# Performance work log

Hardware: AMD Instinct MI355X
Metric: run time of the kernel (lower is better)

The kernel has to match this reference:

```python
import jax, jax.numpy as jnp
import numpy as np

K = 7            # involution kernel size
GC = 16          # group_channels (fixed in module)
BN_EPS = 1e-5


def setup_inputs() -> dict:
    key = jax.random.key(0)
    ks = jax.random.split(key, 9)
    B, C, H, W = 4, 256, 64, 64
    OUT = 256
    CR = C // 4                     # reduction_ratio = 4
    G = C // GC                     # groups = 16
    x = jax.random.normal(ks[0], (B, C, H, W), dtype=jnp.float32)
    # conv1: 1x1 conv C -> C//4, no bias (followed by BN)
    w1 = jax.random.normal(ks[1], (CR, C), dtype=jnp.float32) * (1.0 / np.sqrt(C))
    gamma = jax.random.uniform(ks[2], (CR,), dtype=jnp.float32, minval=0.5, maxval=1.5)
    beta = jax.random.normal(ks[3], (CR,), dtype=jnp.float32) * 0.1
    mean = jax.random.normal(ks[4], (CR,), dtype=jnp.float32) * 0.1
    var = jax.random.uniform(ks[5], (CR,), dtype=jnp.float32, minval=0.5, maxval=1.5)
    # conv2: 1x1 conv C//4 -> K^2 * groups, with bias
    w2 = jax.random.normal(ks[6], (K * K * G, CR), dtype=jnp.float32) * (1.0 / np.sqrt(CR))
    b2 = jax.random.normal(ks[7], (K * K * G,), dtype=jnp.float32) * 0.01
    # pointwise: 1x1 conv C -> OUT, no bias
    wp = jax.random.normal(ks[8], (OUT, C), dtype=jnp.float32) * (1.0 / np.sqrt(C))
    return {"x": x, "w1": w1, "gamma": gamma, "beta": beta, "mean": mean,
            "var": var, "w2": w2, "b2": b2, "wp": wp}


def reference(x, w1, gamma, beta, mean, var, w2, b2, wp):
    b, c, h, w = x.shape
    groups = c // GC
    # weight-generation branch: 1x1 conv -> BN (inference) -> ReLU -> 1x1 conv
    y = jnp.einsum('oc,bchw->bohw', w1, x)
    scale = (gamma * jax.lax.rsqrt(var + BN_EPS))[None, :, None, None]
    y = jax.nn.relu((y - mean[None, :, None, None]) * scale + beta[None, :, None, None])
    wt = jnp.einsum('oc,bchw->bohw', w2, y) + b2[None, :, None, None]
    wt = wt.reshape(b, groups, 1, K * K, h, w)
    # unfold: (b, c*K*K, h, w) with channel-major ordering (matches torch Unfold)
    p = (K - 1) // 2
    patches = jax.lax.conv_general_dilated_patches(
        x, (K, K), (1, 1), ((p, p), (p, p)))
    patches = patches.reshape(b, groups, GC, K * K, h, w)
    out = (wt * patches).sum(axis=3).reshape(b, c, h, w)
    return jnp.einsum('oc,bchw->bohw', wp, out)
```

## Files before the change

kernel.cpp:

```cpp
#include <hip/hip_runtime.h>

typedef __attribute__((ext_vector_type(8))) short bf16x8;
typedef __attribute__((ext_vector_type(4))) float f32x4;
typedef __attribute__((ext_vector_type(8))) _Float16 h16x8;
typedef unsigned short u16;
typedef unsigned int u32;

__device__ __forceinline__ float bf2f(u16 u) {
    u32 x = ((u32)u) << 16;
    return __builtin_bit_cast(float, x);
}
__device__ __forceinline__ u16 f2bf(float f) {
    u32 x = __builtin_bit_cast(u32, f);
    return (u16)((x + 0x7fffu + ((x >> 16) & 1u)) >> 16);
}
__device__ __forceinline__ u16 f2h(float f) {
    _Float16 h = (_Float16)f;
    return __builtin_bit_cast(u16, h);
}
__device__ __forceinline__ u32 bfpair_to_h2(u32 a) {
    float f0 = bf2f((u16)(a & 0xffffu));
    float f1 = bf2f((u16)(a >> 16));
    return (u32)f2h(f0) | ((u32)f2h(f1) << 16);
}

__global__ __launch_bounds__(256) void prep2_k(
    const float* __restrict__ x,
    const float* __restrict__ w1, const float* __restrict__ gamma,
    const float* __restrict__ beta, const float* __restrict__ mean,
    const float* __restrict__ var, const float* __restrict__ w2,
    const float* __restrict__ wp,
    u16* __restrict__ xpk, u16* __restrict__ w1pk, float* __restrict__ b1,
    u16* __restrict__ w2gpk, u16* __restrict__ wppk)
{
    const int t = threadIdx.x;
    const int blk = blockIdx.x;
    if (blk < 2048) {
        const int b = blk >> 9, kg = (blk >> 4) & 31, pb = blk & 15;
        const int pix = pb * 256 + t;
        const float* xb = x + ((size_t)(b * 256 + kg * 8)) * 4096 + pix;
        u16 p[8];
#pragma unroll
        for (int j = 0; j < 8; ++j) p[j] = f2bf(xb[(size_t)j * 4096]);
        uint4 v;
        v.x = (u32)p[0] | ((u32)p[1] << 16);
        v.y = (u32)p[2] | ((u32)p[3] << 16);
        v.z = (u32)p[4] | ((u32)p[5] << 16);
        v.w = (u32)p[6] | ((u32)p[7] << 16);
        *reinterpret_cast<uint4*>(&xpk[(((size_t)b * 32 + kg) * 4096 + pix) * 8]) = v;
        return;
    }
    int idx = (blk - 2048) * 256 + t;
    if (idx < 16384) {
        int kg = idx >> 9, m = (idx >> 3) & 63, j = idx & 7;
        float s = gamma[m] * rsqrtf(var[m] + 1e-5f);
        w1pk[idx] = f2bf(w1[m * 256 + kg * 8 + j] * s);
    } else if (idx < 16448) {
        int o = idx - 16384;
        float s = gamma[o] * rsqrtf(var[o] + 1e-5f);
        b1[o] = beta[o] - mean[o] * s;
    } else if (idx < 81984) {
        int i = idx - 16448;
        int g = i >> 12, kg = (i >> 9) & 7, m = (i >> 3) & 63, j = i & 7;
        w2gpk[i] = (m < 49) ? f2bf(w2[(g * 49 + m) * 64 + kg * 8 + j]) : (u16)0;
    } else if (idx < 147520) {
        int i = idx - 81984;
        int kg = i >> 11, m = (i >> 3) & 255, j = i & 7;
        wppk[i] = f2bf(wp[m * 256 + kg * 8 + j]);
    }
}

__global__ __launch_bounds__(256) void gemm1m_k(
    const u16* __restrict__ xpk, const u16* __restrict__ w1pk,
    const float* __restrict__ b1, u16* __restrict__ ypk)
{
    __shared__ u16 Ws[32 * 64 * 8];
    __shared__ u16 As[2][8 * 64 * 8];

    const int t = threadIdx.x, lane = t & 63, wave = t >> 6;
    const int b = blockIdx.y, n0 = blockIdx.x * 64;
    const int ln = lane & 15, lk = lane >> 4;
    const u16* Ab = xpk + (size_t)b * 32 * 4096 * 8;

    for (int s = t; s < 2048; s += 256) {
        int kg = s >> 6, m = s & 63;
        uint4 v = *reinterpret_cast<const uint4*>(&w1pk[(size_t)s * 8]);
        *reinterpret_cast<uint4*>(&Ws[((kg * 64) + (m ^ (kg & 7))) * 8]) = v;
    }
    uint4 rs[2];
#pragma unroll
    for (int r = 0; r < 2; ++r) {
        int s = r * 256 + t, kg = s >> 6, nn = s & 63;
        rs[r] = *reinterpret_cast<const uint4*>(&Ab[((size_t)kg * 4096 + n0 + nn) * 8]);
    }
#pragma unroll
    for (int r = 0; r < 2; ++r) {
        int s = r * 256 + t, kg = s >> 6, nn = s & 63;
        *reinterpret_cast<uint4*>(&As[0][((kg * 64) + (nn ^ kg)) * 8]) = rs[r];
    }
    __syncthreads();

    f32x4 acc[4];
#pragma unroll
    for (int i = 0; i < 4; ++i)
#pragma unroll
        for (int e = 0; e < 4; ++e) acc[i][e] = 0.f;

    for (int ks = 0; ks < 4; ++ks) {
        const int cur = ks & 1;
        if (ks < 3) {
#pragma unroll
            for (int r = 0; r < 2; ++r) {
                int s = r * 256 + t, kg = s >> 6, nn = s & 63;
                rs[r] = *reinterpret_cast<const uint4*>(
                    &Ab[(((size_t)(ks + 1) * 8 + kg) * 4096 + n0 + nn) * 8]);
            }
        }
#pragma unroll
        for (int k32 = 0; k32 < 2; ++k32) {
            const int kgl = k32 * 4 + lk;
            const int kgw = ks * 8 + kgl;
            bf16x8 a[4];
#pragma unroll
            for (int i = 0; i < 4; ++i) {
                int n = i * 16 + ln;
                a[i] = *reinterpret_cast<const bf16x8*>(
                    &As[cur][((kgl * 64) + (n ^ kgl)) * 8]);
            }
            const int m = wave * 16 + ln;
            const bf16x8 bfr = *reinterpret_cast<const bf16x8*>(
                &Ws[((kgw * 64) + (m ^ (kgw & 7))) * 8]);
#pragma unroll
            for (int i = 0; i < 4; ++i)
                acc[i] = __builtin_amdgcn_mfma_f32_16x16x32_bf16(a[i], bfr, acc[i], 0, 0, 0);
        }
        if (ks < 3) {
#pragma unroll
            for (int r = 0; r < 2; ++r) {
                int s = r * 256 + t, kg = s >> 6, nn = s & 63;
                *reinterpret_cast<uint4*>(
                    &As[cur ^ 1][((kg * 64) + (nn ^ kg)) * 8]) = rs[r];
            }
            __syncthreads();
        }
    }

    const int m = wave * 16 + ln;
    const float bv = b1[m];
    u16* yb = ypk + ((size_t)b * 8 + (m >> 3)) * 4096 * 8 + (m & 7);
#pragma unroll
    for (int i = 0; i < 4; ++i) {
        const int n = n0 + i * 16 + lk * 4;
#pragma unroll
        for (int r = 0; r < 4; ++r)
            yb[(size_t)(n + r) * 8] = f2bf(fmaxf(acc[i][r] + bv, 0.f));
    }
}

__global__ __launch_bounds__(256, 2) void fusedinv_k(
    const u16* __restrict__ ypk, const u16* __restrict__ w2gpk,
    const float* __restrict__ b2, const u16* __restrict__ xpk,
    u16* __restrict__ invpk)
{
    __shared__ alignas(16) char Lds[66560];
    u16* As = (u16*)Lds;
    u16* Ws = (u16*)(Lds + 32768);
    _Float16* xs = (_Float16*)Lds;
    u16* wt16 = (u16*)(Lds + 40960);

    const int t = threadIdx.x, lane = t & 63, wave = t >> 6;
    const int tile = blockIdx.x, g = blockIdx.y, b = blockIdx.z;
    const int ty0 = (tile >> 2) * 16, tx0 = (tile & 3) * 16;
    const int ln = lane & 15, lk = lane >> 4;

    const u16* yb = ypk + (size_t)b * 8 * 4096 * 8;
#pragma unroll
    for (int r = 0; r < 8; ++r) {
        int s = r * 256 + t;
        int kg = s >> 8, n = s & 255;
        int gpix = (ty0 + (n >> 4)) * 64 + tx0 + (n & 15);
        *reinterpret_cast<uint4*>(&As[(size_t)s * 8]) =
            *reinterpret_cast<const uint4*>(&yb[((size_t)kg * 4096 + gpix) * 8]);
    }
#pragma unroll
    for (int r = 0; r < 2; ++r) {
        int s = r * 256 + t;
        *reinterpret_cast<uint4*>(&Ws[(size_t)s * 8]) =
            *reinterpret_cast<const uint4*>(&w2gpk[((size_t)g * 512 + s) * 8]);
    }
    __syncthreads();

    f32x4 acc[16];
#pragma unroll
    for (int i = 0; i < 16; ++i)
#pragma unroll
        for (int e = 0; e < 4; ++e) acc[i][e] = 0.f;

#pragma unroll
    for (int k32 = 0; k32 < 2; ++k32) {
        const int kg = k32 * 4 + lk;
        const bf16x8 wf = *reinterpret_cast<const bf16x8*>(
            &Ws[((kg * 64) + wave * 16 + ln) * 8]);
#pragma unroll
        for (int i = 0; i < 16; ++i) {
            const bf16x8 af = *reinterpret_cast<const bf16x8*>(
                &As[((kg * 256) + i * 16 + ln) * 8]);
            acc[i] = __builtin_amdgcn_mfma_f32_16x16x32_bf16(af, wf, acc[i], 0, 0, 0);
        }
    }
    __syncthreads();

    const int m = wave * 16 + ln;
    if (m < 49) {
        const float bv = b2[g * 49 + m];
#pragma unroll
        for (int i = 0; i < 16; ++i) {
            u16 h0 = f2h(acc[i][0] + bv), h1 = f2h(acc[i][1] + bv);
            u16 h2 = f2h(acc[i][2] + bv), h3 = f2h(acc[i][3] + bv);
            uint2 v;
            v.x = (u32)h0 | ((u32)h1 << 16);
            v.y = (u32)h2 | ((u32)h3 << 16);
            *reinterpret_cast<uint2*>(&wt16[m * 260 + i * 16 + lk * 4]) = v;
        }
    }

    const u16* xb = xpk + ((size_t)b * 32 + g * 2) * 4096 * 8;
    for (int idx = t; idx < 968; idx += 256) {
        int plane = idx & 1, sp = idx >> 1;
        int sy = sp / 22, sx = sp - sy * 22;
        int gy = ty0 + sy - 3, gx = tx0 + sx - 3;
        uint4 v = {0u, 0u, 0u, 0u};
        if ((unsigned)gy < 64u && (unsigned)gx < 64u)
            v = *reinterpret_cast<const uint4*>(
                &xb[((size_t)plane * 4096 + gy * 64 + gx) * 8]);
        uint4 h;
        h.x = bfpair_to_h2(v.x); h.y = bfpair_to_h2(v.y);
        h.z = bfpair_to_h2(v.z); h.w = bfpair_to_h2(v.w);
        *reinterpret_cast<uint4*>(&xs[((size_t)plane * 484 + sp) * 8]) = h;
    }
    __syncthreads();

    const int py = t >> 4, px = t & 15;
    float o[16];
#pragma unroll
    for (int i = 0; i < 16; ++i) o[i] = 0.f;

    for (int dy = 0; dy < 7; ++dy) {
        const int rowb = (py + dy) * 22 + px;
#pragma unroll
        for (int dx = 0; dx < 7; ++dx) {
            const int kk = dy * 7 + dx;
            const float wf = (float)__builtin_bit_cast(_Float16, wt16[kk * 260 + t]);
            const int sp = rowb + dx;
            const h16x8 x0 = *reinterpret_cast<const h16x8*>(&xs[(size_t)sp * 8]);
            const h16x8 x1 = *reinterpret_cast<const h16x8*>(&xs[((size_t)484 + sp) * 8]);
#pragma unroll
            for (int c = 0; c < 8; ++c) {
                o[c]     += wf * (float)x0[c];
                o[8 + c] += wf * (float)x1[c];
            }
        }
    }

    const int pix = (ty0 + py) * 64 + tx0 + px;
#pragma unroll
    for (int h = 0; h < 2; ++h) {
        u16 p[8];
#pragma unroll
        for (int j = 0; j < 8; ++j) p[j] = f2bf(o[h * 8 + j]);
        uint4 v;
        v.x = (u32)p[0] | ((u32)p[1] << 16);
        v.y = (u32)p[2] | ((u32)p[3] << 16);
        v.z = (u32)p[4] | ((u32)p[5] << 16);
        v.w = (u32)p[6] | ((u32)p[7] << 16);
        *reinterpret_cast<uint4*>(
            &invpk[(((size_t)b * 32 + g * 2 + h) * 4096 + pix) * 8]) = v;
    }
}

template<int K, int MP, bool OUT_BF16>
__global__ __launch_bounds__(256) void mgemm_k(
    const u16* __restrict__ Apk,
    const u16* __restrict__ Wpk,
    const float* __restrict__ bias,
    void* __restrict__ Cout,
    int Mout)
{
    constexpr int NK = K / 64;
    constexpr int DB = (NK > 1) ? 2 : 1;
    __shared__ u16 As[DB][8 * 128 * 8];
    __shared__ u16 Ws[(K / 8) * 64 * 8];

    const int t = threadIdx.x;
    const int lane = t & 63, wave = t >> 6;
    const int m0 = blockIdx.x * 64;
    const int batch = blockIdx.y >> 5;
    const int n0 = (blockIdx.y & 31) * 128;
    const u16* Ab = Apk + (size_t)batch * (K / 8) * 4096 * 8;

    const int n0w = (wave & 1) * 64;
    const int m0w = (wave >> 1) * 32;
    const int ln = lane & 15, lk = lane >> 4;

    for (int s = t; s < (K / 8) * 64; s += 256) {
        int kg = s >> 6, m = s & 63;
        const uint4 v = *reinterpret_cast<const uint4*>(
            &Wpk[((size_t)kg * MP + m0 + m) * 8]);
        *reinterpret_cast<uint4*>(&Ws[((size_t)kg * 64 + (m ^ (kg & 7))) * 8]) = v;
    }

    uint4 rs[4];
#pragma unroll
    for (int r = 0; r < 4; ++r) {
        int s = r * 256 + t, kg = s >> 7, nn = s & 127;
        rs[r] = *reinterpret_cast<const uint4*>(&Ab[((size_t)kg * 4096 + n0 + nn) * 8]);
    }
#pragma unroll
    for (int r = 0; r < 4; ++r) {
        int s = r * 256 + t, kg = s >> 7, nn = s & 127;
        *reinterpret_cast<uint4*>(&As[0][((size_t)kg * 128 + (nn ^ kg)) * 8]) = rs[r];
    }
    __syncthreads();

    f32x4 acc[4][2];
#pragma unroll
    for (int i = 0; i < 4; ++i)
#pragma unroll
        for (int f = 0; f < 2; ++f)
#pragma unroll
            for (int e = 0; e < 4; ++e) acc[i][f][e] = 0.f;

    for (int ks = 0; ks < NK; ++ks) {
        const int cur = ks & (DB - 1);
        if (ks + 1 < NK) {
#pragma unroll
            for (int r = 0; r < 4; ++r) {
                int s = r * 256 + t, kg = s >> 7, nn = s & 127;
                rs[r] = *reinterpret_cast<const uint4*>(
                    &Ab[(((size_t)(ks + 1) * 8 + kg) * 4096 + n0 + nn) * 8]);
            }
        }
#pragma unroll
        for (int k32 = 0; k32 < 2; ++k32) {
            const int kg = k32 * 4 + lk;
            bf16x8 a[4], bfr[2];
#pragma unroll
            for (int i = 0; i < 4; ++i) {
                int n = n0w + i * 16 + ln;
                a[i] = *reinterpret_cast<const bf16x8*>(
                    &As[cur][((size_t)kg * 128 + (n ^ kg)) * 8]);
            }
            const int kgw = ks * 8 + kg;
#pragma unroll
            for (int f = 0; f < 2; ++f) {
                int m = m0w + f * 16 + ln;
                bfr[f] = *reinterpret_cast<const bf16x8*>(
                    &Ws[((size_t)kgw * 64 + (m ^ (kgw & 7))) * 8]);
            }
#pragma unroll
            for (int i = 0; i < 4; ++i)
#pragma unroll
                for (int f = 0; f < 2; ++f)
                    acc[i][f] = __builtin_amdgcn_mfma_f32_16x16x32_bf16(
                        a[i], bfr[f], acc[i][f], 0, 0, 0);
        }
        if (ks + 1 < NK) {
#pragma unroll
            for (int r = 0; r < 4; ++r) {
                int s = r * 256 + t, kg = s >> 7, nn = s & 127;
                *reinterpret_cast<uint4*>(
                    &As[cur ^ 1][((size_t)kg * 128 + (nn ^ kg)) * 8]) = rs[r];
            }
            __syncthreads();
        }
    }

#pragma unroll
    for (int f = 0; f < 2; ++f) {
        const int m = m0 + m0w + f * 16 + ln;
        if (m < Mout) {
#pragma unroll
            for (int i = 0; i < 4; ++i) {
                const int n = n0 + n0w + i * 16 + lk * 4;
                const size_t off = ((size_t)batch * Mout + m) * 4096 + n;
                if (OUT_BF16) {
                    const float bv = bias[m];
                    u16 p[4];
#pragma unroll
                    for (int r = 0; r < 4; ++r) p[r] = f2bf(acc[i][f][r] + bv);
                    uint2 v;
                    v.x = (u32)p[0] | ((u32)p[1] << 16);
                    v.y = (u32)p[2] | ((u32)p[3] << 16);
                    *reinterpret_cast<uint2*>(&((u16*)Cout)[off]) = v;
                } else {
                    float4 v = {acc[i][f][0], acc[i][f][1], acc[i][f][2], acc[i][f][3]};
                    *reinterpret_cast<float4*>(&((float*)Cout)[off]) = v;
                }
            }
        }
    }
}

extern "C" void kernel_launch(void* const* d_in, const int* in_sizes, int n_in,
                              void* d_out, int out_size, void* d_ws, size_t ws_size,
                              hipStream_t stream)
{
    const float* x     = (const float*)d_in[0];
    const float* w1    = (const float*)d_in[1];
    const float* gamma = (const float*)d_in[2];
    const float* beta  = (const float*)d_in[3];
    const float* mean  = (const float*)d_in[4];
    const float* var   = (const float*)d_in[5];
    const float* w2    = (const float*)d_in[6];
    const float* b2    = (const float*)d_in[7];
    const float* wp    = (const float*)d_in[8];
    float* out = (float*)d_out;
    float* ws  = (float*)d_ws;

    float* b1 = ws;
    u16* u = (u16*)(ws + 64);
    u16* w1pk  = u;
    u16* w2gpk = u + 16384;
    u16* wppk  = u + 81920;
    u16* xpk   = u + 147456;
    u16* ypk   = u + 4341760;
    u16* invpk = u + 5390336;

    prep2_k<<<2625, 256, 0, stream>>>(x, w1, gamma, beta, mean, var, w2, wp,
                                      xpk, w1pk, b1, w2gpk, wppk);
    gemm1m_k<<<dim3(64, 4), 256, 0, stream>>>(xpk, w1pk, b1, ypk);
    fusedinv_k<<<dim3(16, 16, 4), 256, 0, stream>>>(ypk, w2gpk, b2, xpk, invpk);
    mgemm_k<256, 256, false><<<dim3(4, 128), 256, 0, stream>>>(
        invpk, wppk, nullptr, (void*)out, 256);
}
```

Measured before the change: 49.54 us.

## Fold input and weight prep kernel into consumer kernels, reading fp32 directly

Removes the separate prep kernel that packed x to bf16 and converted and packed the weights. Each consumer now reads fp32 x or weights directly and converts them while staging into LDS, with the BN scale and bias recomputed inline. gemm1m now runs 512 threads arranged as a 4x2 wave grid, so each wave handles half as many columns. This saves a launch and the write and re-read of the packed x tensor, at the cost of redundant weight conversion in every block and strided fp32 gathers of x in both gemm1m and the halo load of fusedinv.

```diff
diff --git a/kernel.cpp b/kernel.cpp
--- a/kernel.cpp
+++ b/kernel.cpp
@@ -6,10 +6,6 @@
 typedef unsigned short u16;
 typedef unsigned int u32;
 
-__device__ __forceinline__ float bf2f(u16 u) {
-    u32 x = ((u32)u) << 16;
-    return __builtin_bit_cast(float, x);
-}
 __device__ __forceinline__ u16 f2bf(float f) {
     u32 x = __builtin_bit_cast(u32, f);
     return (u16)((x + 0x7fffu + ((x >> 16) & 1u)) >> 16);
@@ -18,91 +14,53 @@
     _Float16 h = (_Float16)f;
     return __builtin_bit_cast(u16, h);
 }
-__device__ __forceinline__ u32 bfpair_to_h2(u32 a) {
-    float f0 = bf2f((u16)(a & 0xffffu));
-    float f1 = bf2f((u16)(a >> 16));
-    return (u32)f2h(f0) | ((u32)f2h(f1) << 16);
-}
-
-__global__ __launch_bounds__(256) void prep2_k(
+
+__global__ __launch_bounds__(512) void gemm1m_k(
     const float* __restrict__ x,
     const float* __restrict__ w1, const float* __restrict__ gamma,
     const float* __restrict__ beta, const float* __restrict__ mean,
-    const float* __restrict__ var, const float* __restrict__ w2,
-    const float* __restrict__ wp,
-    u16* __restrict__ xpk, u16* __restrict__ w1pk, float* __restrict__ b1,
-    u16* __restrict__ w2gpk, u16* __restrict__ wppk)
-{
-    const int t = threadIdx.x;
-    const int blk = blockIdx.x;
-    if (blk < 2048) {
-        const int b = blk >> 9, kg = (blk >> 4) & 31, pb = blk & 15;
-        const int pix = pb * 256 + t;
-        const float* xb = x + ((size_t)(b * 256 + kg * 8)) * 4096 + pix;
-        u16 p[8];
-#pragma unroll
-        for (int j = 0; j < 8; ++j) p[j] = f2bf(xb[(size_t)j * 4096]);
-        uint4 v;
-        v.x = (u32)p[0] | ((u32)p[1] << 16);
-        v.y = (u32)p[2] | ((u32)p[3] << 16);
-        v.z = (u32)p[4] | ((u32)p[5] << 16);
-        v.w = (u32)p[6] | ((u32)p[7] << 16);
-        *reinterpret_cast<uint4*>(&xpk[(((size_t)b * 32 + kg) * 4096 + pix) * 8]) = v;
-        return;
-    }
-    int idx = (blk - 2048) * 256 + t;
-    if (idx < 16384) {
-        int kg = idx >> 9, m = (idx >> 3) & 63, j = idx & 7;
-        float s = gamma[m] * rsqrtf(var[m] + 1e-5f);
-        w1pk[idx] = f2bf(w1[m * 256 + kg * 8 + j] * s);
-    } else if (idx < 16448) {
-        int o = idx - 16384;
-        float s = gamma[o] * rsqrtf(var[o] + 1e-5f);
-        b1[o] = beta[o] - mean[o] * s;
-    } else if (idx < 81984) {
-        int i = idx - 16448;
-        int g = i >> 12, kg = (i >> 9) & 7, m = (i >> 3) & 63, j = i & 7;
-        w2gpk[i] = (m < 49) ? f2bf(w2[(g * 49 + m) * 64 + kg * 8 + j]) : (u16)0;
-    } else if (idx < 147520) {
-        int i = idx - 81984;
-        int kg = i >> 11, m = (i >> 3) & 255, j = i & 7;
-        wppk[i] = f2bf(wp[m * 256 + kg * 8 + j]);
-    }
-}
-
-__global__ __launch_bounds__(256) void gemm1m_k(
-    const u16* __restrict__ xpk, const u16* __restrict__ w1pk,
-    const float* __restrict__ b1, u16* __restrict__ ypk)
+    const float* __restrict__ var,
+    u16* __restrict__ ypk)
 {
     __shared__ u16 Ws[32 * 64 * 8];
     __shared__ u16 As[2][8 * 64 * 8];
-
     const int t = threadIdx.x, lane = t & 63, wave = t >> 6;
     const int b = blockIdx.y, n0 = blockIdx.x * 64;
     const int ln = lane & 15, lk = lane >> 4;
-    const u16* Ab = xpk + (size_t)b * 32 * 4096 * 8;
-
-    for (int s = t; s < 2048; s += 256) {
+    const int wm = wave >> 1, wn = wave & 1;
+    const float* xb = x + (size_t)b * 256 * 4096;
+
+    for (int s = t; s < 2048; s += 512) {
         int kg = s >> 6, m = s & 63;
-        uint4 v = *reinterpret_cast<const uint4*>(&w1pk[(size_t)s * 8]);
+        float sc = gamma[m] * rsqrtf(var[m] + 1e-5f);
+        const float4 f0 = *reinterpret_cast<const float4*>(&w1[(size_t)m * 256 + kg * 8]);
+        const float4 f1 = *reinterpret_cast<const float4*>(&w1[(size_t)m * 256 + kg * 8 + 4]);
+        uint4 v;
+        v.x = (u32)f2bf(f0.x * sc) | ((u32)f2bf(f0.y * sc) << 16);
+        v.y = (u32)f2bf(f0.z * sc) | ((u32)f2bf(f0.w * sc) << 16);
+        v.z = (u32)f2bf(f1.x * sc) | ((u32)f2bf(f1.y * sc) << 16);
+        v.w = (u32)f2bf(f1.z * sc) | ((u32)f2bf(f1.w * sc) << 16);
         *reinterpret_cast<uint4*>(&Ws[((kg * 64) + (m ^ (kg & 7))) * 8]) = v;
     }
-    uint4 rs[2];
-#pragma unroll
-    for (int r = 0; r < 2; ++r) {
-        int s = r * 256 + t, kg = s >> 6, nn = s & 63;
-        rs[r] = *reinterpret_cast<const uint4*>(&Ab[((size_t)kg * 4096 + n0 + nn) * 8]);
-    }
-#pragma unroll
-    for (int r = 0; r < 2; ++r) {
-        int s = r * 256 + t, kg = s >> 6, nn = s & 63;
-        *reinterpret_cast<uint4*>(&As[0][((kg * 64) + (nn ^ kg)) * 8]) = rs[r];
-    }
-    __syncthreads();
-
-    f32x4 acc[4];
-#pragma unroll
-    for (int i = 0; i < 4; ++i)
+
+    const int skg = t >> 6, snn = t & 63;
+    float rx[8];
+#pragma unroll
+    for (int j = 0; j < 8; ++j)
+        rx[j] = xb[(size_t)(skg * 8 + j) * 4096 + n0 + snn];
+    {
+        uint4 v;
+        v.x = (u32)f2bf(rx[0]) | ((u32)f2bf(rx[1]) << 16);
+        v.y = (u32)f2bf(rx[2]) | ((u32)f2bf(rx[3]) << 16);
+        v.z = (u32)f2bf(rx[4]) | ((u32)f2bf(rx[5]) << 16);
+        v.w = (u32)f2bf(rx[6]) | ((u32)f2bf(rx[7]) << 16);
+        *reinterpret_cast<uint4*>(&As[0][((skg * 64) + (snn ^ skg)) * 8]) = v;
+    }
+    __syncthreads();
+
+    f32x4 acc[2];
+#pragma unroll
+    for (int i = 0; i < 2; ++i)
 #pragma unroll
         for (int e = 0; e < 4; ++e) acc[i][e] = 0.f;
 
@@ -110,47 +68,45 @@
         const int cur = ks & 1;
         if (ks < 3) {
 #pragma unroll
-            for (int r = 0; r < 2; ++r) {
-                int s = r * 256 + t, kg = s >> 6, nn = s & 63;
-                rs[r] = *reinterpret_cast<const uint4*>(
-                    &Ab[(((size_t)(ks + 1) * 8 + kg) * 4096 + n0 + nn) * 8]);
-            }
+            for (int j = 0; j < 8; ++j)
+                rx[j] = xb[(size_t)((ks + 1) * 64 + skg * 8 + j) * 4096 + n0 + snn];
         }
 #pragma unroll
         for (int k32 = 0; k32 < 2; ++k32) {
             const int kgl = k32 * 4 + lk;
             const int kgw = ks * 8 + kgl;
-            bf16x8 a[4];
-#pragma unroll
-            for (int i = 0; i < 4; ++i) {
-                int n = i * 16 + ln;
+            bf16x8 a[2];
+#pragma unroll
+            for (int i = 0; i < 2; ++i) {
+                int n = wn * 32 + i * 16 + ln;
                 a[i] = *reinterpret_cast<const bf16x8*>(
                     &As[cur][((kgl * 64) + (n ^ kgl)) * 8]);
             }
-            const int m = wave * 16 + ln;
+            const int m = wm * 16 + ln;
             const bf16x8 bfr = *reinterpret_cast<const bf16x8*>(
                 &Ws[((kgw * 64) + (m ^ (kgw & 7))) * 8]);
 #pragma unroll
-            for (int i = 0; i < 4; ++i)
+            for (int i = 0; i < 2; ++i)
                 acc[i] = __builtin_amdgcn_mfma_f32_16x16x32_bf16(a[i], bfr, acc[i], 0, 0, 0);
         }
         if (ks < 3) {
-#pragma unroll
-            for (int r = 0; r < 2; ++r) {
-                int s = r * 256 + t, kg = s >> 6, nn = s & 63;
-                *reinterpret_cast<uint4*>(
-                    &As[cur ^ 1][((kg * 64) + (nn ^ kg)) * 8]) = rs[r];
-            }
+            uint4 v;
+            v.x = (u32)f2bf(rx[0]) | ((u32)f2bf(rx[1]) << 16);
+            v.y = (u32)f2bf(rx[2]) | ((u32)f2bf(rx[3]) << 16);
+            v.z = (u32)f2bf(rx[4]) | ((u32)f2bf(rx[5]) << 16);
+            v.w = (u32)f2bf(rx[6]) | ((u32)f2bf(rx[7]) << 16);
+            *reinterpret_cast<uint4*>(&As[cur ^ 1][((skg * 64) + (snn ^ skg)) * 8]) = v;
             __syncthreads();
         }
     }
 
-    const int m = wave * 16 + ln;
-    const float bv = b1[m];
+    const int m = wm * 16 + ln;
+    const float sc = gamma[m] * rsqrtf(var[m] + 1e-5f);
+    const float bv = beta[m] - mean[m] * sc;
     u16* yb = ypk + ((size_t)b * 8 + (m >> 3)) * 4096 * 8 + (m & 7);
 #pragma unroll
-    for (int i = 0; i < 4; ++i) {
-        const int n = n0 + i * 16 + lk * 4;
+    for (int i = 0; i < 2; ++i) {
+        const int n = n0 + wn * 32 + i * 16 + lk * 4;
 #pragma unroll
         for (int r = 0; r < 4; ++r)
             yb[(size_t)(n + r) * 8] = f2bf(fmaxf(acc[i][r] + bv, 0.f));
@@ -158,8 +114,8 @@
 }
 
 __global__ __launch_bounds__(256, 2) void fusedinv_k(
-    const u16* __restrict__ ypk, const u16* __restrict__ w2gpk,
-    const float* __restrict__ b2, const u16* __restrict__ xpk,
+    const u16* __restrict__ ypk, const float* __restrict__ w2,
+    const float* __restrict__ b2, const float* __restrict__ x,
     u16* __restrict__ invpk)
 {
     __shared__ alignas(16) char Lds[66560];
@@ -185,8 +141,19 @@
 #pragma unroll
     for (int r = 0; r < 2; ++r) {
         int s = r * 256 + t;
-        *reinterpret_cast<uint4*>(&Ws[(size_t)s * 8]) =
-            *reinterpret_cast<const uint4*>(&w2gpk[((size_t)g * 512 + s) * 8]);
+        int kg = s >> 6, m = s & 63;
+        uint4 v = {0u, 0u, 0u, 0u};
+        if (m < 49) {
+            const float4 f0 = *reinterpret_cast<const float4*>(
+                &w2[(size_t)(g * 49 + m) * 64 + kg * 8]);
+            const float4 f1 = *reinterpret_cast<const float4*>(
+                &w2[(size_t)(g * 49 + m) * 64 + kg * 8 + 4]);
+            v.x = (u32)f2bf(f0.x) | ((u32)f2bf(f0.y) << 16);
+            v.y = (u32)f2bf(f0.z) | ((u32)f2bf(f0.w) << 16);
+            v.z = (u32)f2bf(f1.x) | ((u32)f2bf(f1.y) << 16);
+            v.w = (u32)f2bf(f1.z) | ((u32)f2bf(f1.w) << 16);
+        }
+        *reinterpret_cast<uint4*>(&Ws[(size_t)s * 8]) = v;
     }
     __syncthreads();
 
@@ -224,18 +191,22 @@
         }
     }
 
-    const u16* xb = xpk + ((size_t)b * 32 + g * 2) * 4096 * 8;
+    const float* xb = x + (size_t)(b * 256 + g * 16) * 4096;
     for (int idx = t; idx < 968; idx += 256) {
-        int plane = idx & 1, sp = idx >> 1;
+        int plane = idx / 484, sp = idx - plane * 484;
         int sy = sp / 22, sx = sp - sy * 22;
         int gy = ty0 + sy - 3, gx = tx0 + sx - 3;
-        uint4 v = {0u, 0u, 0u, 0u};
-        if ((unsigned)gy < 64u && (unsigned)gx < 64u)
-            v = *reinterpret_cast<const uint4*>(
-                &xb[((size_t)plane * 4096 + gy * 64 + gx) * 8]);
-        uint4 h;
-        h.x = bfpair_to_h2(v.x); h.y = bfpair_to_h2(v.y);
-        h.z = bfpair_to_h2(v.z); h.w = bfpair_to_h2(v.w);
+        uint4 h = {0u, 0u, 0u, 0u};
+        if ((unsigned)gy < 64u && (unsigned)gx < 64u) {
+            const float* xp = &xb[(size_t)(plane * 8) * 4096 + gy * 64 + gx];
+            float f[8];
+#pragma unroll
+            for (int j = 0; j < 8; ++j) f[j] = xp[(size_t)j * 4096];
+            h.x = (u32)f2h(f[0]) | ((u32)f2h(f[1]) << 16);
+            h.y = (u32)f2h(f[2]) | ((u32)f2h(f[3]) << 16);
+            h.z = (u32)f2h(f[4]) | ((u32)f2h(f[5]) << 16);
+            h.w = (u32)f2h(f[6]) | ((u32)f2h(f[7]) << 16);
+        }
         *reinterpret_cast<uint4*>(&xs[((size_t)plane * 484 + sp) * 8]) = h;
     }
     __syncthreads();
@@ -278,34 +249,36 @@
     }
 }
 
-template<int K, int MP, bool OUT_BF16>
-__global__ __launch_bounds__(256) void mgemm_k(
+__global__ __launch_bounds__(256) void mgemm4_k(
     const u16* __restrict__ Apk,
-    const u16* __restrict__ Wpk,
-    const float* __restrict__ bias,
-    void* __restrict__ Cout,
-    int Mout)
+    const float* __restrict__ wp,
+    float* __restrict__ Cout)
 {
-    constexpr int NK = K / 64;
-    constexpr int DB = (NK > 1) ? 2 : 1;
-    __shared__ u16 As[DB][8 * 128 * 8];
-    __shared__ u16 Ws[(K / 8) * 64 * 8];
+    __shared__ u16 As[2][8 * 128 * 8];
+    __shared__ u16 Ws[32 * 64 * 8];
 
     const int t = threadIdx.x;
     const int lane = t & 63, wave = t >> 6;
     const int m0 = blockIdx.x * 64;
     const int batch = blockIdx.y >> 5;
     const int n0 = (blockIdx.y & 31) * 128;
-    const u16* Ab = Apk + (size_t)batch * (K / 8) * 4096 * 8;
+    const u16* Ab = Apk + (size_t)batch * 32 * 4096 * 8;
 
     const int n0w = (wave & 1) * 64;
     const int m0w = (wave >> 1) * 32;
     const int ln = lane & 15, lk = lane >> 4;
 
-    for (int s = t; s < (K / 8) * 64; s += 256) {
+    for (int s = t; s < 2048; s += 256) {
         int kg = s >> 6, m = s & 63;
-        const uint4 v = *reinterpret_cast<const uint4*>(
-            &Wpk[((size_t)kg * MP + m0 + m) * 8]);
+        const float4 f0 = *reinterpret_cast<const float4*>(
+            &wp[(size_t)(m0 + m) * 256 + kg * 8]);
+        const float4 f1 = *reinterpret_cast<const float4*>(
+            &wp[(size_t)(m0 + m) * 256 + kg * 8 + 4]);
+        uint4 v;
+        v.x = (u32)f2bf(f0.x) | ((u32)f2bf(f0.y) << 16);
+        v.y = (u32)f2bf(f0.z) | ((u32)f2bf(f0.w) << 16);
+        v.z = (u32)f2bf(f1.x) | ((u32)f2bf(f1.y) << 16);
+        v.w = (u32)f2bf(f1.z) | ((u32)f2bf(f1.w) << 16);
         *reinterpret_cast<uint4*>(&Ws[((size_t)kg * 64 + (m ^ (kg & 7))) * 8]) = v;
     }
 
@@ -330,9 +303,9 @@
 #pragma unroll
             for (int e = 0; e < 4; ++e) acc[i][f][e] = 0.f;
 
-    for (int ks = 0; ks < NK; ++ks) {
-        const int cur = ks & (DB - 1);
-        if (ks + 1 < NK) {
+    for (int ks = 0; ks < 4; ++ks) {
+        const int cur = ks & 1;
+        if (ks < 3) {
 #pragma unroll
             for (int r = 0; r < 4; ++r) {
                 int s = r * 256 + t, kg = s >> 7, nn = s & 127;
@@ -364,7 +337,7 @@
                     acc[i][f] = __builtin_amdgcn_mfma_f32_16x16x32_bf16(
                         a[i], bfr[f], acc[i][f], 0, 0, 0);
         }
-        if (ks + 1 < NK) {
+        if (ks < 3) {
 #pragma unroll
             for (int r = 0; r < 4; ++r) {
                 int s = r * 256 + t, kg = s >> 7, nn = s & 127;
@@ -378,25 +351,11 @@
 #pragma unroll
     for (int f = 0; f < 2; ++f) {
         const int m = m0 + m0w + f * 16 + ln;
-        if (m < Mout) {
-#pragma unroll
-            for (int i = 0; i < 4; ++i) {
-                const int n = n0 + n0w + i * 16 + lk * 4;
-                const size_t off = ((size_t)batch * Mout + m) * 4096 + n;
-                if (OUT_BF16) {
-                    const float bv = bias[m];
-                    u16 p[4];
-#pragma unroll
-                    for (int r = 0; r < 4; ++r) p[r] = f2bf(acc[i][f][r] + bv);
-                    uint2 v;
-                    v.x = (u32)p[0] | ((u32)p[1] << 16);
-                    v.y = (u32)p[2] | ((u32)p[3] << 16);
-                    *reinterpret_cast<uint2*>(&((u16*)Cout)[off]) = v;
-                } else {
-                    float4 v = {acc[i][f][0], acc[i][f][1], acc[i][f][2], acc[i][f][3]};
-                    *reinterpret_cast<float4*>(&((float*)Cout)[off]) = v;
-                }
-            }
+#pragma unroll
+        for (int i = 0; i < 4; ++i) {
+            const int n = n0 + n0w + i * 16 + lk * 4;
+            float4 v = {acc[i][f][0], acc[i][f][1], acc[i][f][2], acc[i][f][3]};
+            *reinterpret_cast<float4*>(&Cout[((size_t)batch * 256 + m) * 4096 + n]) = v;
         }
     }
 }
@@ -415,21 +374,12 @@
     const float* b2    = (const float*)d_in[7];
     const float* wp    = (const float*)d_in[8];
     float* out = (float*)d_out;
-    float* ws  = (float*)d_ws;
-
-    float* b1 = ws;
-    u16* u = (u16*)(ws + 64);
-    u16* w1pk  = u;
-    u16* w2gpk = u + 16384;
-    u16* wppk  = u + 81920;
-    u16* xpk   = u + 147456;
-    u16* ypk   = u + 4341760;
-    u16* invpk = u + 5390336;
-
-    prep2_k<<<2625, 256, 0, stream>>>(x, w1, gamma, beta, mean, var, w2, wp,
-                                      xpk, w1pk, b1, w2gpk, wppk);
-    gemm1m_k<<<dim3(64, 4), 256, 0, stream>>>(xpk, w1pk, b1, ypk);
-    fusedinv_k<<<dim3(16, 16, 4), 256, 0, stream>>>(ypk, w2gpk, b2, xpk, invpk);
-    mgemm_k<256, 256, false><<<dim3(4, 128), 256, 0, stream>>>(
-        invpk, wppk, nullptr, (void*)out, 256);
-}
+
+    u16* u = (u16*)d_ws;
+    u16* ypk   = u;
+    u16* invpk = u + 1048576;
+
+    gemm1m_k<<<dim3(64, 4), 512, 0, stream>>>(x, w1, gamma, beta, mean, var, ypk);
+    fusedinv_k<<<dim3(16, 16, 4), 256, 0, stream>>>(ypk, w2, b2, x, invpk);
+    mgemm4_k<<<dim3(4, 128), 256, 0, stream>>>(invpk, wp, out);
+}
```

Result: slower. 50.96 us (+2.9%).
